# Optimization experiments

Hardware: AMD Instinct MI355X
Metric: run time of the kernel (lower is better)

## Reference

```python
import jax, jax.numpy as jnp
import numpy as np

D_MODEL = 1024
N_HEADS = 16
D_K = D_MODEL // N_HEADS
D_FF = 4096
EPS = 1e-6


def setup_inputs() -> dict:
    key = jax.random.key(0)
    ks = jax.random.split(key, 12)
    s = 1.0 / np.sqrt(D_MODEL)
    inp = {
        "x": jax.random.normal(ks[0], (4, 2048, D_MODEL), jnp.float32),
        "src_mask": jnp.ones((4, 1, 1, 2048), jnp.int32),
        "Wq": jax.random.normal(ks[1], (D_MODEL, D_MODEL), jnp.float32) * s,
        "bq": jnp.zeros((D_MODEL,), jnp.float32),
        "Wk": jax.random.normal(ks[2], (D_MODEL, D_MODEL), jnp.float32) * s,
        "bk": jnp.zeros((D_MODEL,), jnp.float32),
        "Wv": jax.random.normal(ks[3], (D_MODEL, D_MODEL), jnp.float32) * s,
        "bv": jnp.zeros((D_MODEL,), jnp.float32),
        "Wo": jax.random.normal(ks[4], (D_MODEL, D_MODEL), jnp.float32) * s,
        "bo": jnp.zeros((D_MODEL,), jnp.float32),
        "W1": jax.random.normal(ks[5], (D_MODEL, D_FF), jnp.float32) * s,
        "b1": jnp.zeros((D_FF,), jnp.float32),
        "W2": jax.random.normal(ks[6], (D_FF, D_MODEL), jnp.float32) * (1.0 / np.sqrt(D_FF)),
        "b2": jnp.zeros((D_MODEL,), jnp.float32),
        # scalar LayerNormalization params (alpha=ones(1), bias=zeros(1)) for the 2 residual norms
        "ln1_alpha": jnp.ones((1,), jnp.float32),
        "ln1_bias": jnp.zeros((1,), jnp.float32),
        "ln2_alpha": jnp.ones((1,), jnp.float32),
        "ln2_bias": jnp.zeros((1,), jnp.float32),
    }
    return inp


def _layernorm(x, alpha, bias):
    # matches torch: mean + std (unbiased, ddof=1), (x-mean)/(std+eps)
    mean = jnp.mean(x, axis=-1, keepdims=True)
    std = jnp.std(x, axis=-1, keepdims=True, ddof=1)
    return alpha * ((x - mean) / (std + EPS)) + bias


def _mha(x, mask, Wq, bq, Wk, bk, Wv, bv, Wo, bo):
    B, S, _ = x.shape
    q = (x @ Wq + bq).reshape(B, S, N_HEADS, D_K).transpose(0, 2, 1, 3)
    k = (x @ Wk + bk).reshape(B, S, N_HEADS, D_K).transpose(0, 2, 1, 3)
    v = (x @ Wv + bv).reshape(B, S, N_HEADS, D_K).transpose(0, 2, 1, 3)
    scores = jnp.einsum("bhqd,bhkd->bhqk", q, k) / jnp.sqrt(jnp.float32(D_K))
    scores = jnp.where(mask == 0, jnp.float32(-1e9), scores)
    attn = jax.nn.softmax(scores, axis=-1)
    ctx = jnp.einsum("bhqk,bhkd->bhqd", attn, v)
    ctx = ctx.transpose(0, 2, 1, 3).reshape(B, S, D_MODEL)
    return ctx @ Wo + bo


def reference(x, src_mask, Wq, bq, Wk, bk, Wv, bv, Wo, bo, W1, b1, W2, b2,
              ln1_alpha, ln1_bias, ln2_alpha, ln2_bias):
    # pre-norm residual 1: self-attention
    h = _layernorm(x, ln1_alpha, ln1_bias)
    x = x + _mha(h, src_mask, Wq, bq, Wk, bk, Wv, bv, Wo, bo)
    # pre-norm residual 2: FFN
    h = _layernorm(x, ln2_alpha, ln2_bias)
    ff = jax.nn.relu(h @ W1 + b1) @ W2 + b2
    return x + ff
```

## Files before the change

kernel.cpp:

```cpp
#include <hip/hip_runtime.h>

typedef __attribute__((ext_vector_type(8))) short v8s;
typedef __attribute__((ext_vector_type(8))) unsigned short v8u;
typedef __attribute__((ext_vector_type(4))) unsigned short v4u;
typedef __attribute__((ext_vector_type(4))) float f32x4;

#define DEV __device__ __forceinline__

DEV unsigned short f2bf(float f) {
  union { float f; unsigned u; } v; v.f = f;
  unsigned r = v.u + 0x7fffu + ((v.u >> 16) & 1u);
  return (unsigned short)(r >> 16);
}

DEV void gload16(const unsigned short* g, unsigned short* l) {
  __builtin_amdgcn_global_load_lds(
      (const __attribute__((address_space(1))) unsigned int*)g,
      (__attribute__((address_space(3))) unsigned int*)l, 16, 0, 0);
}

#define SL2E 0.1803368801111204f

__global__ __launch_bounds__(256) void ln_kernel(
    const float* __restrict__ x, unsigned short* __restrict__ h,
    const float* __restrict__ alpha, const float* __restrict__ beta)
{
  int row = blockIdx.x;
  int tid = threadIdx.x;
  const float4* xr = reinterpret_cast<const float4*>(x + (size_t)row * 1024);
  float4 v = xr[tid];
  float s  = v.x + v.y + v.z + v.w;
  float ss = v.x * v.x + v.y * v.y + v.z * v.z + v.w * v.w;
#pragma unroll
  for (int off = 1; off < 64; off <<= 1) {
    s  += __shfl_xor(s, off);
    ss += __shfl_xor(ss, off);
  }
  __shared__ float ps[4][2];
  int wid = tid >> 6, lane = tid & 63;
  if (lane == 0) { ps[wid][0] = s; ps[wid][1] = ss; }
  __syncthreads();
  s  = ps[0][0] + ps[1][0] + ps[2][0] + ps[3][0];
  ss = ps[0][1] + ps[1][1] + ps[2][1] + ps[3][1];
  float mean = s * (1.0f / 1024.0f);
  float var  = (ss - 1024.0f * mean * mean) * (1.0f / 1023.0f);
  float inv  = 1.0f / (sqrtf(fmaxf(var, 0.0f)) + 1e-6f);
  float a = alpha[0], b = beta[0];
  v4u o;
  o[0] = f2bf(a * ((v.x - mean) * inv) + b);
  o[1] = f2bf(a * ((v.y - mean) * inv) + b);
  o[2] = f2bf(a * ((v.z - mean) * inv) + b);
  o[3] = f2bf(a * ((v.w - mean) * inv) + b);
  *reinterpret_cast<v4u*>(h + (size_t)row * 1024 + tid * 4) = o;
}

__global__ __launch_bounds__(256) void transpose_convert(
    const float* __restrict__ W, unsigned short* __restrict__ Wt, int K, int N)
{
  __shared__ float t[32][33];
  int n0 = blockIdx.x * 32, k0 = blockIdx.y * 32;
  int tx = threadIdx.x, ty = threadIdx.y;
#pragma unroll
  for (int i = 0; i < 4; ++i)
    t[ty + i * 8][tx] = W[(size_t)(k0 + ty + i * 8) * N + n0 + tx];
  __syncthreads();
#pragma unroll
  for (int i = 0; i < 4; ++i)
    Wt[(size_t)(n0 + ty + i * 8) * K + k0 + tx] = f2bf(t[tx][ty + i * 8]);
}

enum { MODE_QKV = 0, MODE_RES = 2, MODE_FFN1 = 3 };

#define BUF_ELEMS ((128 + 256) * 64)

DEV void stage_part(const unsigned short* Aptr, const unsigned short* Bptr,
                    unsigned short* buf, int K, int part, int wid, int lane)
{
  {
    int d = (part * 8 + wid) * 64 + lane;
    int r = d >> 3, p = d & 7;
    gload16(Aptr + (size_t)r * K + 8 * (p ^ (r & 7)),
            buf + (size_t)(part * 8 + wid) * 512);
  }
#pragma unroll
  for (int j = 0; j < 2; ++j) {
    int ib = part * 2 + j;
    int d = (ib * 8 + wid) * 64 + lane;
    int r = d >> 3, p = d & 7;
    gload16(Bptr + (size_t)r * K + 8 * (p ^ (r & 7)),
            buf + 128 * 64 + (size_t)(ib * 8 + wid) * 512);
  }
}

template <int MODE>
__global__ __launch_bounds__(512, 2) void gemm_pipe(
    const unsigned short* __restrict__ A, const unsigned short* __restrict__ Bt,
    const float* __restrict__ bias0, const float* __restrict__ bias1,
    const float* __restrict__ bias2, const float* __restrict__ resid,
    void* __restrict__ o0, void* __restrict__ o1, void* __restrict__ o2,
    int M, int N, int K)
{
  __shared__ unsigned short lds[3 * BUF_ELEMS];

  int nbx = M >> 7, nwg = gridDim.x;
  int lin = blockIdx.x;
  int qq = nwg >> 3, rr = nwg & 7;
  int xcd = lin & 7, idx = lin >> 3;
  int swz = (xcd < rr ? xcd * (qq + 1) : rr * (qq + 1) + (xcd - rr) * qq) + idx;
  int bx = swz % nbx, by = swz / nbx;

  int tid = threadIdx.x, lane = tid & 63, wid = tid >> 6;
  int wm = wid >> 2, wn = wid & 3;
  int g = lane >> 4, c0 = lane & 15;
  int rowBase = bx * 128, colBase = by * 256;

  const unsigned short* Ab = A  + (size_t)rowBase * K;
  const unsigned short* Bb = Bt + (size_t)colBase * K;
  int NT = K >> 6;

  f32x4 acc[4][4];
#pragma unroll
  for (int m = 0; m < 4; ++m)
#pragma unroll
    for (int n = 0; n < 4; ++n) acc[m][n] = (f32x4){0.f, 0.f, 0.f, 0.f};

  stage_part(Ab, Bb, lds, K, 0, wid, lane);
  stage_part(Ab, Bb, lds, K, 1, wid, lane);
  stage_part(Ab + 64, Bb + 64, lds + BUF_ELEMS, K, 0, wid, lane);
  stage_part(Ab + 64, Bb + 64, lds + BUF_ELEMS, K, 1, wid, lane);
  asm volatile("s_waitcnt vmcnt(6)" ::: "memory");
  __builtin_amdgcn_s_barrier();
  asm volatile("" ::: "memory");

  int cur = 0;
  for (int t = 0; t < NT; ++t) {
    const char* Abuf = (const char*)(lds + cur * BUF_ELEMS);
    const char* Bbuf = Abuf + 128 * 128;
    int nxt2 = cur + 2; if (nxt2 >= 3) nxt2 -= 3;
    unsigned short* sbuf = lds + nxt2 * BUF_ELEMS;
    bool doStage = (t + 2 < NT);
    int ks_ = (t + 2) << 6;
    int e = (c0 & 7) << 4;

#pragma unroll
    for (int ph = 0; ph < 2; ++ph) {
      v8s af[4], bfr[4];
#pragma unroll
      for (int m = 0; m < 4; ++m)
        af[m] = *reinterpret_cast<const v8s*>(
            Abuf + (wm * 64 + m * 16 + c0) * 128 + ((ph * 64 + g * 16) ^ e));
#pragma unroll
      for (int n = 0; n < 4; ++n)
        bfr[n] = *reinterpret_cast<const v8s*>(
            Bbuf + (wn * 64 + n * 16 + c0) * 128 + ((ph * 64 + g * 16) ^ e));

      if (doStage) stage_part(Ab + ks_, Bb + ks_, sbuf, K, ph, wid, lane);

      __builtin_amdgcn_s_setprio(1);
#pragma unroll
      for (int m = 0; m < 4; ++m)
#pragma unroll
        for (int n = 0; n < 4; ++n)
          acc[m][n] = __builtin_amdgcn_mfma_f32_16x16x32_bf16(
              af[m], bfr[n], acc[m][n], 0, 0, 0);
      __builtin_amdgcn_s_setprio(0);
    }

    if (doStage)            asm volatile("s_waitcnt vmcnt(6)" ::: "memory");
    else if (t + 1 < NT)    asm volatile("s_waitcnt vmcnt(0)" ::: "memory");
    __builtin_amdgcn_sched_barrier(0);
    __builtin_amdgcn_s_barrier();
    asm volatile("" ::: "memory");
    cur = cur + 1; if (cur >= 3) cur -= 3;
  }

#pragma unroll
  for (int mf = 0; mf < 4; ++mf) {
#pragma unroll
    for (int nf = 0; nf < 4; ++nf) {
#pragma unroll
      for (int r = 0; r < 4; ++r) {
        int row = rowBase + wm * 64 + mf * 16 + g * 4 + r;
        int col = colBase + wn * 64 + nf * 16 + c0;
        float v = acc[mf][nf][r];
        if constexpr (MODE == MODE_QKV) {
          int sect = colBase >> 10;
          int cs = col & 1023;
          const float* bp = sect == 0 ? bias0 : (sect == 1 ? bias1 : bias2);
          v += bp[cs];
          int hh = cs >> 6, d = cs & 63;
          int b = row >> 11, sI = row & 2047;
          size_t bh = (size_t)(b * 16 + hh);
          if (sect == 0) {
            ((unsigned short*)o0)[(bh * 2048 + sI) * 64 + d] = f2bf(v * SL2E);
          } else if (sect == 1) {
            ((unsigned short*)o1)[(bh * 2048 + sI) * 64 + d] = f2bf(v);
          } else {
            int k6 = sI & 63;
            int slot = ((k6 >> 5) << 5) | (((k6 >> 2) & 3) << 3) |
                       (((k6 >> 4) & 1) << 2) | (k6 & 3);
            int e2 = slot ^ ((d & 7) << 3);
            ((unsigned short*)o2)[((bh * 32 + (sI >> 6)) * 64 + d) * 64 + e2] = f2bf(v);
          }
        } else if constexpr (MODE == MODE_RES) {
          v += bias0[col];
          ((float*)o0)[(size_t)row * N + col] = resid[(size_t)row * N + col] + v;
        } else {
          v += bias0[col];
          ((unsigned short*)o0)[(size_t)row * N + col] = f2bf(fmaxf(v, 0.0f));
        }
      }
    }
  }
}

__global__ __launch_bounds__(512, 1) void gemm_ffn1_256(
    const unsigned short* __restrict__ A, const unsigned short* __restrict__ Bt,
    const float* __restrict__ bias, unsigned short* __restrict__ out,
    int M, int N, int K)
{
  __shared__ unsigned short lds[2][512 * 64];

  int nbx = M >> 8, nwg = gridDim.x;
  int lin = blockIdx.x;
  int qq = nwg >> 3, rr = nwg & 7;
  int xcd = lin & 7, idx = lin >> 3;
  int swz = (xcd < rr ? xcd * (qq + 1) : rr * (qq + 1) + (xcd - rr) * qq) + idx;
  int bx = swz % nbx, by = swz / nbx;

  int tid = threadIdx.x, lane = tid & 63, wid = tid >> 6;
  int wm = wid >> 2, wn = wid & 3;
  int g = lane >> 4, c0 = lane & 15;
  int rowBase = bx * 256, colBase = by * 256;

  const unsigned short* Ab = A  + (size_t)rowBase * K;
  const unsigned short* Bb = Bt + (size_t)colBase * K;
  int NT = K >> 6;

  const unsigned short* src[8]; int dq[8];
#pragma unroll
  for (int i = 0; i < 8; ++i) {
    int q = i * 512 + tid;
    dq[i] = q;
    if (i < 4) {
      int r = q >> 3, p = q & 7;
      src[i] = Ab + (size_t)r * K + 8 * (p ^ (r & 7));
    } else {
      int qb2 = q - 2048, r = qb2 >> 3, p = qb2 & 7;
      src[i] = Bb + (size_t)r * K + 8 * (p ^ (r & 7));
    }
  }

  f32x4 acc[8][4];
#pragma unroll
  for (int m = 0; m < 8; ++m)
#pragma unroll
    for (int n = 0; n < 4; ++n) acc[m][n] = (f32x4){0.f, 0.f, 0.f, 0.f};

#define STG256(tt, lo, hi) do { \
    unsigned short* sb_ = &lds[(tt) & 1][0]; int ko_ = (tt) << 6; \
    _Pragma("unroll") for (int i = lo; i < hi; ++i) gload16(src[i] + ko_, sb_ + dq[i] * 8); \
  } while (0)

  STG256(0, 0, 8);
  asm volatile("s_waitcnt vmcnt(0)" ::: "memory");
  __builtin_amdgcn_s_barrier();
  asm volatile("" ::: "memory");

  for (int t = 0; t < NT; ++t) {
    const char* buf = (const char*)&lds[t & 1][0];
    bool more = (t + 1 < NT);
    int e = (c0 & 7) << 4;

#pragma unroll
    for (int ph = 0; ph < 2; ++ph) {
      v8s af[8], bfr[4];
#pragma unroll
      for (int m = 0; m < 8; ++m) {
        int row = wm * 128 + m * 16 + c0;
        af[m] = *reinterpret_cast<const v8s*>(
            buf + row * 128 + ((ph * 64 + g * 16) ^ ((row & 7) << 4)));
      }
#pragma unroll
      for (int n = 0; n < 4; ++n) {
        int row = wn * 64 + n * 16 + c0;
        bfr[n] = *reinterpret_cast<const v8s*>(
            buf + 32768 + row * 128 + ((ph * 64 + g * 16) ^ ((row & 7) << 4)));
      }

      if (more) { if (ph == 0) STG256(t + 1, 0, 4); else STG256(t + 1, 4, 8); }

      __builtin_amdgcn_s_setprio(1);
#pragma unroll
      for (int m = 0; m < 8; ++m)
#pragma unroll
        for (int n = 0; n < 4; ++n)
          acc[m][n] = __builtin_amdgcn_mfma_f32_16x16x32_bf16(
              af[m], bfr[n], acc[m][n], 0, 0, 0);
      __builtin_amdgcn_s_setprio(0);
    }

    if (more) asm volatile("s_waitcnt vmcnt(0)" ::: "memory");
    __builtin_amdgcn_sched_barrier(0);
    __builtin_amdgcn_s_barrier();
    asm volatile("" ::: "memory");
  }
#undef STG256

#pragma unroll
  for (int mf = 0; mf < 8; ++mf) {
#pragma unroll
    for (int nf = 0; nf < 4; ++nf) {
#pragma unroll
      for (int r = 0; r < 4; ++r) {
        int row = rowBase + wm * 128 + mf * 16 + g * 4 + r;
        int col = colBase + wn * 64 + nf * 16 + c0;
        float v = acc[mf][nf][r] + bias[col];
        out[(size_t)row * N + col] = f2bf(fmaxf(v, 0.0f));
      }
    }
  }
}

__global__ __launch_bounds__(256) void attn_kernel(
    const unsigned short* __restrict__ q, const unsigned short* __restrict__ k,
    const unsigned short* __restrict__ vP, const int* __restrict__ mask,
    unsigned short* __restrict__ ctx)
{
  const int S = 2048, DK = 64, NT = 32;
  int bh = blockIdx.x;
  int b = bh >> 4, hh = bh & 15;
  int qbase = blockIdx.y * 128;
  int tid = threadIdx.x, lane = tid & 63, wid = tid >> 6;
  int g = lane >> 4, c0 = lane & 15;

  __shared__ unsigned short Ks[3 * 4096];
  __shared__ unsigned short Vs[3 * 4096];
  __shared__ unsigned short Mb[2048];

  const unsigned short* qb  = q  + (size_t)bh * S * DK;
  const unsigned short* kb  = k  + (size_t)bh * S * DK;
  const unsigned short* vPb = vP + (size_t)bh * 32 * 4096;
  const int* mb = mask + b * S;

  const int4* mb4 = reinterpret_cast<const int4*>(mb);
  int4 ma = mb4[tid * 2], mc = mb4[tid * 2 + 1];
  unsigned short bneg = f2bf(-1e9f);
  v8u bw;
  bw[0] = ma.x ? 0 : bneg; bw[1] = ma.y ? 0 : bneg;
  bw[2] = ma.z ? 0 : bneg; bw[3] = ma.w ? 0 : bneg;
  bw[4] = mc.x ? 0 : bneg; bw[5] = mc.y ? 0 : bneg;
  bw[6] = mc.z ? 0 : bneg; bw[7] = mc.w ? 0 : bneg;
  *reinterpret_cast<v8u*>(&Mb[tid * 8]) = bw;
  int ok = (ma.x && ma.y && ma.z && ma.w && mc.x && mc.y && mc.z && mc.w) ? 1 : 0;
  int allValid = __syncthreads_and(ok);

  int qrow = qbase + wid * 32 + c0;
  v8s aq[2][2];
#pragma unroll
  for (int s = 0; s < 2; ++s)
#pragma unroll
    for (int t = 0; t < 2; ++t)
      aq[s][t] = *reinterpret_cast<const v8s*>(
          &qb[(size_t)(qrow + s * 16) * DK + t * 32 + g * 8]);

  int i0 = tid, i1 = tid + 256;
  int r0 = i0 >> 3, m0 = i0 & 7;
  int r1 = i1 >> 3, m1 = i1 & 7;
  const unsigned short* ks0 = kb + (size_t)r0 * DK + 8 * (m0 ^ (r0 & 7));
  const unsigned short* ks1 = kb + (size_t)r1 * DK + 8 * (m1 ^ (r1 & 7));

  f32x4 acc[2][4];
#pragma unroll
  for (int s = 0; s < 2; ++s)
#pragma unroll
    for (int no = 0; no < 4; ++no) acc[s][no] = (f32x4){0.f, 0.f, 0.f, 0.f};
  float lsum0 = 0.f, lsum1 = 0.f;

#define ASTAGE(bi, tt) do { \
    unsigned short* kd = Ks + (bi) * 4096; unsigned short* vd = Vs + (bi) * 4096; \
    int ko = (tt) * 64 * DK; \
    gload16(ks0 + ko, kd + i0 * 8); gload16(ks1 + ko, kd + i1 * 8); \
    gload16(vPb + (tt) * 4096 + i0 * 8, vd + i0 * 8); \
    gload16(vPb + (tt) * 4096 + i1 * 8, vd + i1 * 8); \
  } while (0)

  ASTAGE(0, 0);
  ASTAGE(1, 1);
  asm volatile("s_waitcnt vmcnt(4)" ::: "memory");
  __builtin_amdgcn_s_barrier();
  asm volatile("" ::: "memory");

  int cur = 0, nx2 = 2;
  for (int t = 0; t < NT; ++t) {
    bool more2 = (t + 2 < NT);
    if (more2) ASTAGE(nx2, t + 2);
    const unsigned short* Kc = Ks + cur * 4096;
    const unsigned short* Vc = Vs + cur * 4096;

    float p0[16], p1[16];
#pragma unroll
    for (int n = 0; n < 4; ++n) {
      int kvr = n * 16 + c0;
      const char* krow = (const char*)(Kc + kvr * DK);
      int sw = (kvr & 7) << 4;
      v8s ak0 = *reinterpret_cast<const v8s*>(krow + ((g * 16) ^ sw));
      v8s ak1 = *reinterpret_cast<const v8s*>(krow + ((64 + g * 16) ^ sw));
      f32x4 s0 = (f32x4){0.f, 0.f, 0.f, 0.f};
      f32x4 s1 = (f32x4){0.f, 0.f, 0.f, 0.f};
      s0 = __builtin_amdgcn_mfma_f32_16x16x32_bf16(ak0, aq[0][0], s0, 0, 0, 0);
      s0 = __builtin_amdgcn_mfma_f32_16x16x32_bf16(ak1, aq[0][1], s0, 0, 0, 0);
      s1 = __builtin_amdgcn_mfma_f32_16x16x32_bf16(ak0, aq[1][0], s1, 0, 0, 0);
      s1 = __builtin_amdgcn_mfma_f32_16x16x32_bf16(ak1, aq[1][1], s1, 0, 0, 0);
#pragma unroll
      for (int r = 0; r < 4; ++r) { p0[n * 4 + r] = s0[r]; p1[n * 4 + r] = s1[r]; }
    }
    if (!allValid) {
#pragma unroll
      for (int n = 0; n < 4; ++n) {
        v4u mbv = *reinterpret_cast<const v4u*>(&Mb[t * 64 + n * 16 + g * 4]);
#pragma unroll
        for (int r = 0; r < 4; ++r) {
          union { unsigned u; float f; } cv; cv.u = ((unsigned)mbv[r]) << 16;
          p0[n * 4 + r] += cv.f; p1[n * 4 + r] += cv.f;
        }
      }
    }

    float ts0 = 0.f, ts1 = 0.f;
#pragma unroll
    for (int i = 0; i < 16; ++i) {
      p0[i] = exp2f(p0[i]); ts0 += p0[i];
      p1[i] = exp2f(p1[i]); ts1 += p1[i];
    }
    lsum0 += ts0; lsum1 += ts1;

    v8s pb0[2], pb1[2];
#pragma unroll
    for (int c = 0; c < 2; ++c) {
      union { v8s s; unsigned u[4]; } k0, k1;
#pragma unroll
      for (int hp = 0; hp < 4; ++hp) {
        asm("v_cvt_pk_bf16_f32 %0, %1, %2"
            : "=v"(k0.u[hp]) : "v"(p0[c * 8 + 2 * hp]), "v"(p0[c * 8 + 2 * hp + 1]));
        asm("v_cvt_pk_bf16_f32 %0, %1, %2"
            : "=v"(k1.u[hp]) : "v"(p1[c * 8 + 2 * hp]), "v"(p1[c * 8 + 2 * hp + 1]));
      }
      pb0[c] = k0.s; pb1[c] = k1.s;
    }

#pragma unroll
    for (int c = 0; c < 2; ++c) {
#pragma unroll
      for (int no = 0; no < 4; ++no) {
        int d = no * 16 + c0;
        v8s av = *reinterpret_cast<const v8s*>(
            (const char*)(Vc + d * 64) + ((c * 64 + g * 16) ^ ((d & 7) << 4)));
        acc[0][no] = __builtin_amdgcn_mfma_f32_16x16x32_bf16(av, pb0[c], acc[0][no], 0, 0, 0);
        acc[1][no] = __builtin_amdgcn_mfma_f32_16x16x32_bf16(av, pb1[c], acc[1][no], 0, 0, 0);
      }
    }

    if (more2)              asm volatile("s_waitcnt vmcnt(4)" ::: "memory");
    else if (t + 1 < NT)    asm volatile("s_waitcnt vmcnt(0)" ::: "memory");
    __builtin_amdgcn_sched_barrier(0);
    __builtin_amdgcn_s_barrier();
    asm volatile("" ::: "memory");
    cur = (cur + 1 < 3) ? cur + 1 : 0;
    nx2 = (nx2 + 1 < 3) ? nx2 + 1 : 0;
  }
#undef ASTAGE

  lsum0 += __shfl_xor(lsum0, 16); lsum0 += __shfl_xor(lsum0, 32);
  lsum1 += __shfl_xor(lsum1, 16); lsum1 += __shfl_xor(lsum1, 32);
  float lrow[2] = {lsum0, lsum1};

#pragma unroll
  for (int s = 0; s < 2; ++s) {
    float inv = 1.0f / fmaxf(lrow[s], 1e-30f);
#pragma unroll
    for (int no = 0; no < 4; ++no) {
      v4u o;
      o[0] = f2bf(acc[s][no][0] * inv);
      o[1] = f2bf(acc[s][no][1] * inv);
      o[2] = f2bf(acc[s][no][2] * inv);
      o[3] = f2bf(acc[s][no][3] * inv);
      *reinterpret_cast<v4u*>(
          &ctx[(size_t)(b * S + qrow + s * 16) * 1024 + hh * 64 + no * 16 + g * 4]) = o;
    }
  }
}

extern "C" void kernel_launch(void* const* d_in, const int* in_sizes, int n_in,
                              void* d_out, int out_size, void* d_ws, size_t ws_size,
                              hipStream_t stream)
{
  (void)in_sizes; (void)n_in; (void)out_size; (void)ws_size;
  const float* x    = (const float*)d_in[0];
  const int*   mask = (const int*)d_in[1];
  const float* Wq = (const float*)d_in[2];  const float* bq = (const float*)d_in[3];
  const float* Wk = (const float*)d_in[4];  const float* bk = (const float*)d_in[5];
  const float* Wv = (const float*)d_in[6];  const float* bv = (const float*)d_in[7];
  const float* Wo = (const float*)d_in[8];  const float* bo = (const float*)d_in[9];
  const float* W1 = (const float*)d_in[10]; const float* b1 = (const float*)d_in[11];
  const float* W2 = (const float*)d_in[12]; const float* b2 = (const float*)d_in[13];
  const float* ln1a = (const float*)d_in[14]; const float* ln1b = (const float*)d_in[15];
  const float* ln2a = (const float*)d_in[16]; const float* ln2b = (const float*)d_in[17];

  char* ws = (char*)d_ws;
  const size_t MB = (size_t)1 << 20;
  unsigned short* wqkvT = (unsigned short*)(ws + 0 * MB);
  unsigned short* woT = (unsigned short*)(ws + 6 * MB);
  unsigned short* w1T = (unsigned short*)(ws + 8 * MB);
  unsigned short* w2T = (unsigned short*)(ws + 16 * MB);
  unsigned short* hb  = (unsigned short*)(ws + 24 * MB);
  unsigned short* qb  = (unsigned short*)(ws + 40 * MB);
  unsigned short* kb  = (unsigned short*)(ws + 56 * MB);
  unsigned short* vPb = (unsigned short*)(ws + 72 * MB);
  unsigned short* ctx = (unsigned short*)(ws + 88 * MB);
  unsigned short* gb  = (unsigned short*)(ws + 40 * MB);
  float* xout = (float*)d_out;

  dim3 tb(32, 8);
  transpose_convert<<<dim3(32, 32),  tb, 0, stream>>>(Wq, wqkvT,               1024, 1024);
  transpose_convert<<<dim3(32, 32),  tb, 0, stream>>>(Wk, wqkvT + 1024 * 1024, 1024, 1024);
  transpose_convert<<<dim3(32, 32),  tb, 0, stream>>>(Wv, wqkvT + 2048 * 1024, 1024, 1024);
  transpose_convert<<<dim3(32, 32),  tb, 0, stream>>>(Wo, woT, 1024, 1024);
  transpose_convert<<<dim3(128, 32), tb, 0, stream>>>(W1, w1T, 1024, 4096);
  transpose_convert<<<dim3(32, 128), tb, 0, stream>>>(W2, w2T, 4096, 1024);

  ln_kernel<<<8192, 256, 0, stream>>>(x, hb, ln1a, ln1b);

  gemm_pipe<MODE_QKV><<<768, 512, 0, stream>>>(
      hb, wqkvT, bq, bk, bv, nullptr, qb, kb, vPb, 8192, 3072, 1024);

  attn_kernel<<<dim3(64, 16), 256, 0, stream>>>(qb, kb, vPb, mask, ctx);

  gemm_pipe<MODE_RES><<<256, 512, 0, stream>>>(
      ctx, woT, bo, nullptr, nullptr, x, xout, nullptr, nullptr, 8192, 1024, 1024);

  ln_kernel<<<8192, 256, 0, stream>>>(xout, hb, ln2a, ln2b);

  gemm_ffn1_256<<<512, 512, 0, stream>>>(hb, w1T, b1, gb, 8192, 4096, 1024);

  gemm_pipe<MODE_RES><<<256, 512, 0, stream>>>(
      gb, w2T, b2, nullptr, nullptr, xout, xout, nullptr, nullptr, 8192, 1024, 4096);
}
```

Baseline: 429.5 us.

## Use 256x256 tile GEMM for QKV, unify FFN1 path, use raw v_exp_f32

The QKV projection moves from the 128x256 triple-buffered kernel to a templated 256x256 double-buffered kernel, which is shared with FFN1. This raises data reuse per block and halves the grid size. The residual GEMMs get a dedicated non-templated kernel. In attention, exp2f is replaced by the raw v_exp_f32 instruction and the K/V staging address math is simplified. FFN1 now issues its next-tile loads all at once before compute rather than split across the two phases, which may hurt overlap.

```diff
diff --git a/kernel.cpp b/kernel.cpp
--- a/kernel.cpp
+++ b/kernel.cpp
@@ -11,6 +11,10 @@
   union { float f; unsigned u; } v; v.f = f;
   unsigned r = v.u + 0x7fffu + ((v.u >> 16) & 1u);
   return (unsigned short)(r >> 16);
+}
+
+DEV float fexp2(float x) {
+  float r; asm("v_exp_f32 %0, %1" : "=v"(r) : "v"(x)); return r;
 }
 
 DEV void gload16(const unsigned short* g, unsigned short* l) {
@@ -71,38 +75,17 @@
 
 enum { MODE_QKV = 0, MODE_RES = 2, MODE_FFN1 = 3 };
 
-#define BUF_ELEMS ((128 + 256) * 64)
-
-DEV void stage_part(const unsigned short* Aptr, const unsigned short* Bptr,
-                    unsigned short* buf, int K, int part, int wid, int lane)
-{
-  {
-    int d = (part * 8 + wid) * 64 + lane;
-    int r = d >> 3, p = d & 7;
-    gload16(Aptr + (size_t)r * K + 8 * (p ^ (r & 7)),
-            buf + (size_t)(part * 8 + wid) * 512);
-  }
-#pragma unroll
-  for (int j = 0; j < 2; ++j) {
-    int ib = part * 2 + j;
-    int d = (ib * 8 + wid) * 64 + lane;
-    int r = d >> 3, p = d & 7;
-    gload16(Bptr + (size_t)r * K + 8 * (p ^ (r & 7)),
-            buf + 128 * 64 + (size_t)(ib * 8 + wid) * 512);
-  }
-}
-
 template <int MODE>
-__global__ __launch_bounds__(512, 2) void gemm_pipe(
+__global__ __launch_bounds__(512, 1) void gemm_256(
     const unsigned short* __restrict__ A, const unsigned short* __restrict__ Bt,
     const float* __restrict__ bias0, const float* __restrict__ bias1,
-    const float* __restrict__ bias2, const float* __restrict__ resid,
+    const float* __restrict__ bias2,
     void* __restrict__ o0, void* __restrict__ o1, void* __restrict__ o2,
     int M, int N, int K)
 {
-  __shared__ unsigned short lds[3 * BUF_ELEMS];
-
-  int nbx = M >> 7, nwg = gridDim.x;
+  __shared__ unsigned short lds[2][512 * 64];
+
+  int nbx = M >> 8, nwg = gridDim.x;
   int lin = blockIdx.x;
   int qq = nwg >> 3, rr = nwg & 7;
   int xcd = lin & 7, idx = lin >> 3;
@@ -112,53 +95,67 @@
   int tid = threadIdx.x, lane = tid & 63, wid = tid >> 6;
   int wm = wid >> 2, wn = wid & 3;
   int g = lane >> 4, c0 = lane & 15;
-  int rowBase = bx * 128, colBase = by * 256;
+  int rowBase = bx * 256, colBase = by * 256;
 
   const unsigned short* Ab = A  + (size_t)rowBase * K;
   const unsigned short* Bb = Bt + (size_t)colBase * K;
   int NT = K >> 6;
 
-  f32x4 acc[4][4];
-#pragma unroll
-  for (int m = 0; m < 4; ++m)
+  const unsigned short* src[8]; int dq[8];
+#pragma unroll
+  for (int i = 0; i < 8; ++i) {
+    int q = i * 512 + tid;
+    dq[i] = q;
+    if (i < 4) {
+      int r = q >> 3, p = q & 7;
+      src[i] = Ab + (size_t)r * K + 8 * (p ^ (r & 7));
+    } else {
+      int qb2 = q - 2048, r = qb2 >> 3, p = qb2 & 7;
+      src[i] = Bb + (size_t)r * K + 8 * (p ^ (r & 7));
+    }
+  }
+
+  f32x4 acc[8][4];
+#pragma unroll
+  for (int m = 0; m < 8; ++m)
 #pragma unroll
     for (int n = 0; n < 4; ++n) acc[m][n] = (f32x4){0.f, 0.f, 0.f, 0.f};
 
-  stage_part(Ab, Bb, lds, K, 0, wid, lane);
-  stage_part(Ab, Bb, lds, K, 1, wid, lane);
-  stage_part(Ab + 64, Bb + 64, lds + BUF_ELEMS, K, 0, wid, lane);
-  stage_part(Ab + 64, Bb + 64, lds + BUF_ELEMS, K, 1, wid, lane);
-  asm volatile("s_waitcnt vmcnt(6)" ::: "memory");
+#define STG256(tt) do { \
+    unsigned short* sb_ = &lds[(tt) & 1][0]; int ko_ = (tt) << 6; \
+    _Pragma("unroll") for (int i = 0; i < 8; ++i) gload16(src[i] + ko_, sb_ + dq[i] * 8); \
+  } while (0)
+
+  STG256(0);
+  asm volatile("s_waitcnt vmcnt(0)" ::: "memory");
   __builtin_amdgcn_s_barrier();
   asm volatile("" ::: "memory");
 
-  int cur = 0;
   for (int t = 0; t < NT; ++t) {
-    const char* Abuf = (const char*)(lds + cur * BUF_ELEMS);
-    const char* Bbuf = Abuf + 128 * 128;
-    int nxt2 = cur + 2; if (nxt2 >= 3) nxt2 -= 3;
-    unsigned short* sbuf = lds + nxt2 * BUF_ELEMS;
-    bool doStage = (t + 2 < NT);
-    int ks_ = (t + 2) << 6;
+    const char* buf = (const char*)&lds[t & 1][0];
+    bool more = (t + 1 < NT);
+    if (more) STG256(t + 1);
     int e = (c0 & 7) << 4;
 
 #pragma unroll
     for (int ph = 0; ph < 2; ++ph) {
-      v8s af[4], bfr[4];
-#pragma unroll
-      for (int m = 0; m < 4; ++m)
+      v8s af[8], bfr[4];
+#pragma unroll
+      for (int m = 0; m < 8; ++m) {
+        int row = wm * 128 + m * 16 + c0;
         af[m] = *reinterpret_cast<const v8s*>(
-            Abuf + (wm * 64 + m * 16 + c0) * 128 + ((ph * 64 + g * 16) ^ e));
-#pragma unroll
-      for (int n = 0; n < 4; ++n)
+            buf + row * 128 + ((ph * 64 + g * 16) ^ e));
+      }
+#pragma unroll
+      for (int n = 0; n < 4; ++n) {
+        int row = wn * 64 + n * 16 + c0;
         bfr[n] = *reinterpret_cast<const v8s*>(
-            Bbuf + (wn * 64 + n * 16 + c0) * 128 + ((ph * 64 + g * 16) ^ e));
-
-      if (doStage) stage_part(Ab + ks_, Bb + ks_, sbuf, K, ph, wid, lane);
+            buf + 32768 + row * 128 + ((ph * 64 + g * 16) ^ e));
+      }
 
       __builtin_amdgcn_s_setprio(1);
 #pragma unroll
-      for (int m = 0; m < 4; ++m)
+      for (int m = 0; m < 8; ++m)
 #pragma unroll
         for (int n = 0; n < 4; ++n)
           acc[m][n] = __builtin_amdgcn_mfma_f32_16x16x32_bf16(
@@ -166,21 +163,20 @@
       __builtin_amdgcn_s_setprio(0);
     }
 
-    if (doStage)            asm volatile("s_waitcnt vmcnt(6)" ::: "memory");
-    else if (t + 1 < NT)    asm volatile("s_waitcnt vmcnt(0)" ::: "memory");
+    if (more) asm volatile("s_waitcnt vmcnt(0)" ::: "memory");
     __builtin_amdgcn_sched_barrier(0);
     __builtin_amdgcn_s_barrier();
     asm volatile("" ::: "memory");
-    cur = cur + 1; if (cur >= 3) cur -= 3;
-  }
-
-#pragma unroll
-  for (int mf = 0; mf < 4; ++mf) {
+  }
+#undef STG256
+
+#pragma unroll
+  for (int mf = 0; mf < 8; ++mf) {
 #pragma unroll
     for (int nf = 0; nf < 4; ++nf) {
 #pragma unroll
       for (int r = 0; r < 4; ++r) {
-        int row = rowBase + wm * 64 + mf * 16 + g * 4 + r;
+        int row = rowBase + wm * 128 + mf * 16 + g * 4 + r;
         int col = colBase + wn * 64 + nf * 16 + c0;
         float v = acc[mf][nf][r];
         if constexpr (MODE == MODE_QKV) {
@@ -202,9 +198,6 @@
             int e2 = slot ^ ((d & 7) << 3);
             ((unsigned short*)o2)[((bh * 32 + (sI >> 6)) * 64 + d) * 64 + e2] = f2bf(v);
           }
-        } else if constexpr (MODE == MODE_RES) {
-          v += bias0[col];
-          ((float*)o0)[(size_t)row * N + col] = resid[(size_t)row * N + col] + v;
         } else {
           v += bias0[col];
           ((unsigned short*)o0)[(size_t)row * N + col] = f2bf(fmaxf(v, 0.0f));
@@ -214,14 +207,35 @@
   }
 }
 
-__global__ __launch_bounds__(512, 1) void gemm_ffn1_256(
+#define BUF_ELEMS ((128 + 256) * 64)
+
+DEV void stage_part(const unsigned short* Aptr, const unsigned short* Bptr,
+                    unsigned short* buf, int K, int part, int wid, int lane)
+{
+  {
+    int d = (part * 8 + wid) * 64 + lane;
+    int r = d >> 3, p = d & 7;
+    gload16(Aptr + (size_t)r * K + 8 * (p ^ (r & 7)),
+            buf + (size_t)(part * 8 + wid) * 512);
+  }
+#pragma unroll
+  for (int j = 0; j < 2; ++j) {
+    int ib = part * 2 + j;
+    int d = (ib * 8 + wid) * 64 + lane;
+    int r = d >> 3, p = d & 7;
+    gload16(Bptr + (size_t)r * K + 8 * (p ^ (r & 7)),
+            buf + 128 * 64 + (size_t)(ib * 8 + wid) * 512);
+  }
+}
+
+__global__ __launch_bounds__(512, 2) void gemm_pipe_res(
     const unsigned short* __restrict__ A, const unsigned short* __restrict__ Bt,
-    const float* __restrict__ bias, unsigned short* __restrict__ out,
-    int M, int N, int K)
-{
-  __shared__ unsigned short lds[2][512 * 64];
-
-  int nbx = M >> 8, nwg = gridDim.x;
+    const float* __restrict__ bias0, const float* __restrict__ resid,
+    float* __restrict__ o0, int M, int N, int K)
+{
+  __shared__ unsigned short lds[3 * BUF_ELEMS];
+
+  int nbx = M >> 7, nwg = gridDim.x;
   int lin = blockIdx.x;
   int qq = nwg >> 3, rr = nwg & 7;
   int xcd = lin & 7, idx = lin >> 3;
@@ -231,68 +245,53 @@
   int tid = threadIdx.x, lane = tid & 63, wid = tid >> 6;
   int wm = wid >> 2, wn = wid & 3;
   int g = lane >> 4, c0 = lane & 15;
-  int rowBase = bx * 256, colBase = by * 256;
+  int rowBase = bx * 128, colBase = by * 256;
 
   const unsigned short* Ab = A  + (size_t)rowBase * K;
   const unsigned short* Bb = Bt + (size_t)colBase * K;
   int NT = K >> 6;
 
-  const unsigned short* src[8]; int dq[8];
-#pragma unroll
-  for (int i = 0; i < 8; ++i) {
-    int q = i * 512 + tid;
-    dq[i] = q;
-    if (i < 4) {
-      int r = q >> 3, p = q & 7;
-      src[i] = Ab + (size_t)r * K + 8 * (p ^ (r & 7));
-    } else {
-      int qb2 = q - 2048, r = qb2 >> 3, p = qb2 & 7;
-      src[i] = Bb + (size_t)r * K + 8 * (p ^ (r & 7));
-    }
-  }
-
-  f32x4 acc[8][4];
-#pragma unroll
-  for (int m = 0; m < 8; ++m)
+  f32x4 acc[4][4];
+#pragma unroll
+  for (int m = 0; m < 4; ++m)
 #pragma unroll
     for (int n = 0; n < 4; ++n) acc[m][n] = (f32x4){0.f, 0.f, 0.f, 0.f};
 
-#define STG256(tt, lo, hi) do { \
-    unsigned short* sb_ = &lds[(tt) & 1][0]; int ko_ = (tt) << 6; \
-    _Pragma("unroll") for (int i = lo; i < hi; ++i) gload16(src[i] + ko_, sb_ + dq[i] * 8); \
-  } while (0)
-
-  STG256(0, 0, 8);
-  asm volatile("s_waitcnt vmcnt(0)" ::: "memory");
+  stage_part(Ab, Bb, lds, K, 0, wid, lane);
+  stage_part(Ab, Bb, lds, K, 1, wid, lane);
+  stage_part(Ab + 64, Bb + 64, lds + BUF_ELEMS, K, 0, wid, lane);
+  stage_part(Ab + 64, Bb + 64, lds + BUF_ELEMS, K, 1, wid, lane);
+  asm volatile("s_waitcnt vmcnt(6)" ::: "memory");
   __builtin_amdgcn_s_barrier();
   asm volatile("" ::: "memory");
 
+  int cur = 0;
   for (int t = 0; t < NT; ++t) {
-    const char* buf = (const char*)&lds[t & 1][0];
-    bool more = (t + 1 < NT);
+    const char* Abuf = (const char*)(lds + cur * BUF_ELEMS);
+    const char* Bbuf = Abuf + 128 * 128;
+    int nxt2 = cur + 2; if (nxt2 >= 3) nxt2 -= 3;
+    unsigned short* sbuf = lds + nxt2 * BUF_ELEMS;
+    bool doStage = (t + 2 < NT);
+    int ks_ = (t + 2) << 6;
     int e = (c0 & 7) << 4;
 
 #pragma unroll
     for (int ph = 0; ph < 2; ++ph) {
-      v8s af[8], bfr[4];
-#pragma unroll
-      for (int m = 0; m < 8; ++m) {
-        int row = wm * 128 + m * 16 + c0;
+      v8s af[4], bfr[4];
+#pragma unroll
+      for (int m = 0; m < 4; ++m)
         af[m] = *reinterpret_cast<const v8s*>(
-            buf + row * 128 + ((ph * 64 + g * 16) ^ ((row & 7) << 4)));
-      }
-#pragma unroll
-      for (int n = 0; n < 4; ++n) {
-        int row = wn * 64 + n * 16 + c0;
+            Abuf + (wm * 64 + m * 16 + c0) * 128 + ((ph * 64 + g * 16) ^ e));
+#pragma unroll
+      for (int n = 0; n < 4; ++n)
         bfr[n] = *reinterpret_cast<const v8s*>(
-            buf + 32768 + row * 128 + ((ph * 64 + g * 16) ^ ((row & 7) << 4)));
-      }
-
-      if (more) { if (ph == 0) STG256(t + 1, 0, 4); else STG256(t + 1, 4, 8); }
+            Bbuf + (wn * 64 + n * 16 + c0) * 128 + ((ph * 64 + g * 16) ^ e));
+
+      if (doStage) stage_part(Ab + ks_, Bb + ks_, sbuf, K, ph, wid, lane);
 
       __builtin_amdgcn_s_setprio(1);
 #pragma unroll
-      for (int m = 0; m < 8; ++m)
+      for (int m = 0; m < 4; ++m)
 #pragma unroll
         for (int n = 0; n < 4; ++n)
           acc[m][n] = __builtin_amdgcn_mfma_f32_16x16x32_bf16(
@@ -300,23 +299,24 @@
       __builtin_amdgcn_s_setprio(0);
     }
 
-    if (more) asm volatile("s_waitcnt vmcnt(0)" ::: "memory");
+    if (doStage)            asm volatile("s_waitcnt vmcnt(6)" ::: "memory");
+    else if (t + 1 < NT)    asm volatile("s_waitcnt vmcnt(0)" ::: "memory");
     __builtin_amdgcn_sched_barrier(0);
     __builtin_amdgcn_s_barrier();
     asm volatile("" ::: "memory");
-  }
-#undef STG256
-
-#pragma unroll
-  for (int mf = 0; mf < 8; ++mf) {
+    cur = cur + 1; if (cur >= 3) cur -= 3;
+  }
+
+#pragma unroll
+  for (int mf = 0; mf < 4; ++mf) {
 #pragma unroll
     for (int nf = 0; nf < 4; ++nf) {
 #pragma unroll
       for (int r = 0; r < 4; ++r) {
-        int row = rowBase + wm * 128 + mf * 16 + g * 4 + r;
+        int row = rowBase + wm * 64 + mf * 16 + g * 4 + r;
         int col = colBase + wn * 64 + nf * 16 + c0;
-        float v = acc[mf][nf][r] + bias[col];
-        out[(size_t)row * N + col] = f2bf(fmaxf(v, 0.0f));
+        float v = acc[mf][nf][r] + bias0[col];
+        o0[(size_t)row * N + col] = resid[(size_t)row * N + col] + v;
       }
     }
   }
@@ -367,8 +367,8 @@
   int i0 = tid, i1 = tid + 256;
   int r0 = i0 >> 3, m0 = i0 & 7;
   int r1 = i1 >> 3, m1 = i1 & 7;
-  const unsigned short* ks0 = kb + (size_t)r0 * DK + 8 * (m0 ^ (r0 & 7));
-  const unsigned short* ks1 = kb + (size_t)r1 * DK + 8 * (m1 ^ (r1 & 7));
+  int ko0 = r0 * DK + 8 * (m0 ^ (r0 & 7));
+  int ko1 = r1 * DK + 8 * (m1 ^ (r1 & 7));
 
   f32x4 acc[2][4];
 #pragma unroll
@@ -378,11 +378,11 @@
   float lsum0 = 0.f, lsum1 = 0.f;
 
 #define ASTAGE(bi, tt) do { \
-    unsigned short* kd = Ks + (bi) * 4096; unsigned short* vd = Vs + (bi) * 4096; \
-    int ko = (tt) * 64 * DK; \
-    gload16(ks0 + ko, kd + i0 * 8); gload16(ks1 + ko, kd + i1 * 8); \
-    gload16(vPb + (tt) * 4096 + i0 * 8, vd + i0 * 8); \
-    gload16(vPb + (tt) * 4096 + i1 * 8, vd + i1 * 8); \
+    int tb_ = (tt) * 4096; \
+    gload16(kb + tb_ + ko0, Ks + (bi) * 4096 + i0 * 8); \
+    gload16(kb + tb_ + ko1, Ks + (bi) * 4096 + i1 * 8); \
+    gload16(vPb + tb_ + i0 * 8, Vs + (bi) * 4096 + i0 * 8); \
+    gload16(vPb + tb_ + i1 * 8, Vs + (bi) * 4096 + i1 * 8); \
   } while (0)
 
   ASTAGE(0, 0);
@@ -430,8 +430,8 @@
     float ts0 = 0.f, ts1 = 0.f;
 #pragma unroll
     for (int i = 0; i < 16; ++i) {
-      p0[i] = exp2f(p0[i]); ts0 += p0[i];
-      p1[i] = exp2f(p1[i]); ts1 += p1[i];
+      p0[i] = fexp2(p0[i]); ts0 += p0[i];
+      p1[i] = fexp2(p1[i]); ts1 += p1[i];
     }
     lsum0 += ts0; lsum1 += ts1;
 
@@ -531,18 +531,17 @@
 
   ln_kernel<<<8192, 256, 0, stream>>>(x, hb, ln1a, ln1b);
 
-  gemm_pipe<MODE_QKV><<<768, 512, 0, stream>>>(
-      hb, wqkvT, bq, bk, bv, nullptr, qb, kb, vPb, 8192, 3072, 1024);
+  gemm_256<MODE_QKV><<<384, 512, 0, stream>>>(
+      hb, wqkvT, bq, bk, bv, qb, kb, vPb, 8192, 3072, 1024);
 
   attn_kernel<<<dim3(64, 16), 256, 0, stream>>>(qb, kb, vPb, mask, ctx);
 
-  gemm_pipe<MODE_RES><<<256, 512, 0, stream>>>(
-      ctx, woT, bo, nullptr, nullptr, x, xout, nullptr, nullptr, 8192, 1024, 1024);
+  gemm_pipe_res<<<256, 512, 0, stream>>>(ctx, woT, bo, x, xout, 8192, 1024, 1024);
 
   ln_kernel<<<8192, 256, 0, stream>>>(xout, hb, ln2a, ln2b);
 
-  gemm_ffn1_256<<<512, 512, 0, stream>>>(hb, w1T, b1, gb, 8192, 4096, 1024);
-
-  gemm_pipe<MODE_RES><<<256, 512, 0, stream>>>(
-      gb, w2T, b2, nullptr, nullptr, xout, xout, nullptr, nullptr, 8192, 1024, 4096);
-}
+  gemm_256<MODE_FFN1><<<512, 512, 0, stream>>>(
+      hb, w1T, b1, nullptr, nullptr, gb, nullptr, nullptr, 8192, 4096, 1024);
+
+  gemm_pipe_res<<<256, 512, 0, stream>>>(gb, w2T, b2, xout, xout, 8192, 1024, 4096);
+}
```

Measured after the change: 401.4 us. 6.5% less time.
